# Kernel optimization log

Measured on AMD Instinct MI355X. Metric: run time of the kernel, lower is better.

## Reference

```python
import jax, jax.numpy as jnp
import numpy as np

B, E, H = 32768, 512, 512


def setup_inputs() -> dict:
    key = jax.random.key(0)
    ks = jax.random.split(key, 7)
    s_e = 1.0 / np.sqrt(E)
    s_h = 1.0 / np.sqrt(H)
    return {
        "input": jax.random.normal(ks[0], (B, E), jnp.float32),
        "h0": jax.random.normal(ks[1], (B, H), jnp.float32),
        "c0": jax.random.normal(ks[2], (B, H), jnp.float32),
        # stacked weights, gate order [i, f, o, g]
        "W_x": jax.random.uniform(ks[3], (4, H, E), jnp.float32, -s_e, s_e),
        "b_x": jax.random.uniform(ks[4], (4, H), jnp.float32, -s_e, s_e),
        "W_h": jax.random.uniform(ks[5], (4, H, H), jnp.float32, -s_h, s_h),
        "b_h": jax.random.uniform(ks[6], (4, H), jnp.float32, -s_h, s_h),
    }


def reference(input, h0, c0, W_x, b_x, W_h, b_h):
    # Fused: two GEMMs over stacked gate weights, then elementwise gate math.
    # z: [4, B, H]; gate order i, f, o, g
    z = (jnp.einsum('be,khe->kbh', input, W_x) + b_x[:, None, :]
         + jnp.einsum('bh,kgh->kbg', h0, W_h) + b_h[:, None, :])
    i = jax.nn.sigmoid(z[0])
    f = jax.nn.sigmoid(z[1])
    o = jax.nn.sigmoid(z[2])
    g = jnp.tanh(z[3])
    c1 = f * c0 + i * g
    h1 = o * jnp.tanh(c1)
    return (h1, c1)
```

## Files before the change

kernel.cpp:

```cpp
#include <hip/hip_runtime.h>


#define BQ 32768
#define HQ 512
#define KK 1024
#define BH (32768 * 512)

typedef __bf16 bf16x8 __attribute__((ext_vector_type(8)));
typedef float f32x4 __attribute__((ext_vector_type(4)));

__device__ __forceinline__ unsigned short f2bf(float f) {
    unsigned int u = __float_as_uint(f);
    unsigned int r = (u + 0x7fffu + ((u >> 16) & 1u)) >> 16;
    return (unsigned short)r;
}

__device__ __forceinline__ void gld_lds16(const unsigned short* g, unsigned short* l) {
    __builtin_amdgcn_global_load_lds(
        (const __attribute__((address_space(1))) void*)g,
        (__attribute__((address_space(3))) void*)l,
        16, 0, 0);
}

__device__ __forceinline__ bf16x8 cvt8(f32x4 a, f32x4 b) {
    bf16x8 w;
    w[0] = (__bf16)a[0]; w[1] = (__bf16)a[1]; w[2] = (__bf16)a[2]; w[3] = (__bf16)a[3];
    w[4] = (__bf16)b[0]; w[5] = (__bf16)b[1]; w[6] = (__bf16)b[2]; w[7] = (__bf16)b[3];
    return w;
}


__global__ __launch_bounds__(256) void pack_W(const float* __restrict__ Wx,
                                              const float* __restrict__ Wh,
                                              const float* __restrict__ bx,
                                              const float* __restrict__ bh,
                                              unsigned short* __restrict__ Wint,
                                              float* __restrict__ biasc) {
    int j = blockIdx.x * 256 + threadIdx.x;
    int c = j >> 8;
    int kc = (j & 255) * 4;
    int gate = (c >> 4) & 3;
    int h = ((c >> 6) << 4) + (c & 15);
    const float* src = (kc < 512)
        ? (Wx + ((size_t)gate * 512 + h) * 512 + kc)
        : (Wh + ((size_t)gate * 512 + h) * 512 + (kc - 512));
    float4 v = *(const float4*)src;
    ushort4 o;
    o.x = f2bf(v.x); o.y = f2bf(v.y); o.z = f2bf(v.z); o.w = f2bf(v.w);
    *(ushort4*)&Wint[(size_t)c * 1024 + kc] = o;
    if ((j & 255) == 0) biasc[c] = bx[gate * 512 + h] + bh[gate * 512 + h];
}


__global__ __launch_bounds__(256, 4) void lstm_gemm(const float* __restrict__ xin,
                                                    const float* __restrict__ hin,
                                                    const unsigned short* __restrict__ Wint,
                                                    const float* __restrict__ biasc,
                                                    const float* __restrict__ c0,
                                                    float* __restrict__ out) {
    __shared__ __align__(16) unsigned short ldsA[128 * 32];
    __shared__ __align__(16) unsigned short ldsB[128 * 32];

    const int tid = threadIdx.x;
    const int lane = tid & 63;
    const int wave = tid >> 6;
    const int wm = wave >> 1;
    const int wn = wave & 1;
    const int quad = lane >> 4;
    const int lrow = lane & 15;

    const int bn = blockIdx.x;
    const int bm = blockIdx.y;
    const int m0 = bm * 128;
    const int n0 = bn * 128;

    const int arow = tid >> 1;
    const int ahalf = tid & 1;
    const int aswz = (arow >> 1) & 3;
    const float* gAx = xin + (size_t)(m0 + arow) * HQ + ahalf * 16;
    const float* gAh = hin + (size_t)(m0 + arow) * HQ + ahalf * 16;
    unsigned short* wA0 = &ldsA[arow * 32 + (((ahalf * 2 + 0) ^ aswz) * 8)];
    unsigned short* wA1 = &ldsA[arow * 32 + (((ahalf * 2 + 1) ^ aswz) * 8)];

    const int brow = tid >> 2;
    const int bunit = (tid & 3) ^ ((tid >> 3) & 3);
    const unsigned short* gB = Wint + (size_t)(n0 + brow) * KK + bunit * 8;

    const int koff = (quad ^ ((lrow >> 1) & 3)) * 8;

    f32x4 acc[4][4];
    for (int i = 0; i < 4; i++)
        for (int j = 0; j < 4; j++) {
            f32x4 z = {0.f, 0.f, 0.f, 0.f};
            acc[i][j] = z;
        }

    f32x4 r0 = *(const f32x4*)(gAx + 0);
    f32x4 r1 = *(const f32x4*)(gAx + 4);
    f32x4 r2 = *(const f32x4*)(gAx + 8);
    f32x4 r3 = *(const f32x4*)(gAx + 12);

    for (int kt = 0; kt < KK; kt += 32) {
        gld_lds16(gB + kt, &ldsB[tid * 8]);
        gld_lds16(gB + (size_t)64 * KK + kt, &ldsB[2048 + tid * 8]);
        *(bf16x8*)wA0 = cvt8(r0, r1);
        *(bf16x8*)wA1 = cvt8(r2, r3);
        __syncthreads();

        const int kn = kt + 32;
        if (kn < KK) {
            const float* p = (kn < 512) ? (gAx + kn) : (gAh + (kn - 512));
            r0 = *(const f32x4*)(p + 0);
            r1 = *(const f32x4*)(p + 4);
            r2 = *(const f32x4*)(p + 8);
            r3 = *(const f32x4*)(p + 12);
        }

        bf16x8 af[4], bfr[4];
        for (int mi = 0; mi < 4; mi++)
            af[mi] = *(const bf16x8*)&ldsA[(wm * 64 + mi * 16 + lrow) * 32 + koff];
        for (int ni = 0; ni < 4; ni++)
            bfr[ni] = *(const bf16x8*)&ldsB[(wn * 64 + ni * 16 + lrow) * 32 + koff];
        for (int mi = 0; mi < 4; mi++)
            for (int ni = 0; ni < 4; ni++)
                acc[mi][ni] = __builtin_amdgcn_mfma_f32_16x16x32_bf16(
                    af[mi], bfr[ni], acc[mi][ni], 0, 0, 0);
        __syncthreads();
    }

    float bi[4];
    for (int ni = 0; ni < 4; ni++)
        bi[ni] = biasc[n0 + wn * 64 + ni * 16 + lrow];
    const int h = (bn * 2 + wn) * 16 + lrow;

    for (int mi = 0; mi < 4; mi++) {
        for (int r = 0; r < 4; r++) {
            int b = m0 + wm * 64 + mi * 16 + quad * 4 + r;
            float zi = acc[mi][0][r] + bi[0];
            float zf = acc[mi][1][r] + bi[1];
            float zo = acc[mi][2][r] + bi[2];
            float zg = acc[mi][3][r] + bi[3];
            float ig = 1.f / (1.f + __expf(-zi));
            float fg = 1.f / (1.f + __expf(-zf));
            float og = 1.f / (1.f + __expf(-zo));
            float gg = 1.f - 2.f / (__expf(2.f * zg) + 1.f);
            float c0v = c0[(size_t)b * HQ + h];
            float c1 = fg * c0v + ig * gg;
            float th = 1.f - 2.f / (__expf(2.f * c1) + 1.f);
            out[(size_t)b * HQ + h] = og * th;
            out[(size_t)BH + (size_t)b * HQ + h] = c1;
        }
    }
}

extern "C" void kernel_launch(void* const* d_in, const int* in_sizes, int n_in,
                              void* d_out, int out_size, void* d_ws, size_t ws_size,
                              hipStream_t stream) {
    (void)in_sizes; (void)n_in; (void)out_size; (void)ws_size;
    const float* input = (const float*)d_in[0];
    const float* h0    = (const float*)d_in[1];
    const float* c0    = (const float*)d_in[2];
    const float* Wx    = (const float*)d_in[3];
    const float* bx    = (const float*)d_in[4];
    const float* Wh    = (const float*)d_in[5];
    const float* bh    = (const float*)d_in[6];
    float* out = (float*)d_out;

    char* ws = (char*)d_ws;
    unsigned short* Wint = (unsigned short*)ws;
    float* biasc = (float*)(ws + (size_t)4 * 1024 * 1024);

    pack_W<<<2048, 256, 0, stream>>>(Wx, Wh, bx, bh, Wint, biasc);
    lstm_gemm<<<dim3(16, 256), 256, 0, stream>>>(input, h0, Wint, biasc, c0, out);
}
```

Baseline: 503.3 us.

## Double-buffer LDS tiles with one barrier per step and remap block order

Converts the GEMM main loop to double-buffered LDS, with a two-stage register prefetch of the fp32 A tile and async B loads into the alternate buffer. Each k-step now needs a single barrier, guarded by explicit waitcnt, so global loads overlap the MFMA work. The launch also changes to a 1D grid with an index remap that spreads M blocks across an interleaved order, which is meant to improve L2 reuse of the weight tiles. In exchange it doubles LDS use, adds register pressure from two A staging sets, and relies on hand-counted vmcnt values being correct.

After: 544.5 us. 1.08x slower.

```diff
diff --git a/kernel.cpp b/kernel.cpp
--- a/kernel.cpp
+++ b/kernel.cpp
@@ -27,6 +27,16 @@
     w[0] = (__bf16)a[0]; w[1] = (__bf16)a[1]; w[2] = (__bf16)a[2]; w[3] = (__bf16)a[3];
     w[4] = (__bf16)b[0]; w[5] = (__bf16)b[1]; w[6] = (__bf16)b[2]; w[7] = (__bf16)b[3];
     return w;
+}
+
+struct AR { f32x4 a, b, c, d; };
+
+__device__ __forceinline__ void loadA(const float* gAx, const float* gAh, int kt, AR& s) {
+    const float* p = (kt < 512) ? (gAx + kt) : (gAh + (kt - 512));
+    s.a = *(const f32x4*)(p + 0);
+    s.b = *(const f32x4*)(p + 4);
+    s.c = *(const f32x4*)(p + 8);
+    s.d = *(const f32x4*)(p + 12);
 }
 
 
@@ -58,8 +68,8 @@
                                                     const float* __restrict__ biasc,
                                                     const float* __restrict__ c0,
                                                     float* __restrict__ out) {
-    __shared__ __align__(16) unsigned short ldsA[128 * 32];
-    __shared__ __align__(16) unsigned short ldsB[128 * 32];
+    __shared__ __align__(16) unsigned short ldsA[2][128 * 32];
+    __shared__ __align__(16) unsigned short ldsB[2][128 * 32];
 
     const int tid = threadIdx.x;
     const int lane = tid & 63;
@@ -69,8 +79,10 @@
     const int quad = lane >> 4;
     const int lrow = lane & 15;
 
-    const int bn = blockIdx.x;
-    const int bm = blockIdx.y;
+    const int bid = blockIdx.x;
+    const int l = bid >> 3;
+    const int bm = (bid & 7) * 32 + (l >> 4);
+    const int bn = l & 15;
     const int m0 = bm * 128;
     const int n0 = bn * 128;
 
@@ -79,8 +91,8 @@
     const int aswz = (arow >> 1) & 3;
     const float* gAx = xin + (size_t)(m0 + arow) * HQ + ahalf * 16;
     const float* gAh = hin + (size_t)(m0 + arow) * HQ + ahalf * 16;
-    unsigned short* wA0 = &ldsA[arow * 32 + (((ahalf * 2 + 0) ^ aswz) * 8)];
-    unsigned short* wA1 = &ldsA[arow * 32 + (((ahalf * 2 + 1) ^ aswz) * 8)];
+    const int wa0 = arow * 32 + (((ahalf * 2 + 0) ^ aswz) * 8);
+    const int wa1 = arow * 32 + (((ahalf * 2 + 1) ^ aswz) * 8);
 
     const int brow = tid >> 2;
     const int bunit = (tid & 3) ^ ((tid >> 3) & 3);
@@ -95,37 +107,56 @@
             acc[i][j] = z;
         }
 
-    f32x4 r0 = *(const f32x4*)(gAx + 0);
-    f32x4 r1 = *(const f32x4*)(gAx + 4);
-    f32x4 r2 = *(const f32x4*)(gAx + 8);
-    f32x4 r3 = *(const f32x4*)(gAx + 12);
-
-    for (int kt = 0; kt < KK; kt += 32) {
-        gld_lds16(gB + kt, &ldsB[tid * 8]);
-        gld_lds16(gB + (size_t)64 * KK + kt, &ldsB[2048 + tid * 8]);
-        *(bf16x8*)wA0 = cvt8(r0, r1);
-        *(bf16x8*)wA1 = cvt8(r2, r3);
-        __syncthreads();
-
-        const int kn = kt + 32;
-        if (kn < KK) {
-            const float* p = (kn < 512) ? (gAx + kn) : (gAh + (kn - 512));
-            r0 = *(const f32x4*)(p + 0);
-            r1 = *(const f32x4*)(p + 4);
-            r2 = *(const f32x4*)(p + 8);
-            r3 = *(const f32x4*)(p + 12);
-        }
-
+    AR s0, s1;
+
+    loadA(gAx, gAh, 0, s0);
+    gld_lds16(gB, &ldsB[0][tid * 8]);
+    gld_lds16(gB + (size_t)64 * KK, &ldsB[0][2048 + tid * 8]);
+    *(bf16x8*)&ldsA[0][wa0] = cvt8(s0.a, s0.b);
+    *(bf16x8*)&ldsA[0][wa1] = cvt8(s0.c, s0.d);
+    loadA(gAx, gAh, 32, s1);
+    asm volatile("s_waitcnt vmcnt(4) lgkmcnt(0)" ::: "memory");
+    __builtin_amdgcn_s_barrier();
+
+#define STEP(I, CUR, WREG, LREG) do {                                          \
+    const int ktn_ = ((I) + 1) * 32;                                           \
+    gld_lds16(gB + ktn_, &ldsB[(CUR) ^ 1][tid * 8]);                           \
+    gld_lds16(gB + (size_t)64 * KK + ktn_, &ldsB[(CUR) ^ 1][2048 + tid * 8]);  \
+    bf16x8 af[4], bfr[4];                                                      \
+    for (int mi = 0; mi < 4; mi++)                                             \
+        af[mi] = *(const bf16x8*)&ldsA[CUR][(wm * 64 + mi * 16 + lrow) * 32 + koff]; \
+    for (int ni = 0; ni < 4; ni++)                                             \
+        bfr[ni] = *(const bf16x8*)&ldsB[CUR][(wn * 64 + ni * 16 + lrow) * 32 + koff]; \
+    *(bf16x8*)&ldsA[(CUR) ^ 1][wa0] = cvt8(WREG.a, WREG.b);                    \
+    *(bf16x8*)&ldsA[(CUR) ^ 1][wa1] = cvt8(WREG.c, WREG.d);                    \
+    int kt2_ = ((I) + 2) * 32;                                                 \
+    if (kt2_ >= KK) kt2_ = KK - 32;                                            \
+    loadA(gAx, gAh, kt2_, LREG);                                               \
+    for (int mi = 0; mi < 4; mi++)                                             \
+        for (int ni = 0; ni < 4; ni++)                                         \
+            acc[mi][ni] = __builtin_amdgcn_mfma_f32_16x16x32_bf16(             \
+                af[mi], bfr[ni], acc[mi][ni], 0, 0, 0);                        \
+    asm volatile("s_waitcnt vmcnt(4) lgkmcnt(0)" ::: "memory");                \
+    __builtin_amdgcn_s_barrier();                                              \
+} while (0)
+
+    for (int ii = 0; ii < 15; ++ii) {
+        STEP(2 * ii + 0, 0, s1, s0);
+        STEP(2 * ii + 1, 1, s0, s1);
+    }
+    STEP(30, 0, s1, s0);
+#undef STEP
+
+    {
         bf16x8 af[4], bfr[4];
         for (int mi = 0; mi < 4; mi++)
-            af[mi] = *(const bf16x8*)&ldsA[(wm * 64 + mi * 16 + lrow) * 32 + koff];
+            af[mi] = *(const bf16x8*)&ldsA[1][(wm * 64 + mi * 16 + lrow) * 32 + koff];
         for (int ni = 0; ni < 4; ni++)
-            bfr[ni] = *(const bf16x8*)&ldsB[(wn * 64 + ni * 16 + lrow) * 32 + koff];
+            bfr[ni] = *(const bf16x8*)&ldsB[1][(wn * 64 + ni * 16 + lrow) * 32 + koff];
         for (int mi = 0; mi < 4; mi++)
             for (int ni = 0; ni < 4; ni++)
                 acc[mi][ni] = __builtin_amdgcn_mfma_f32_16x16x32_bf16(
                     af[mi], bfr[ni], acc[mi][ni], 0, 0, 0);
-        __syncthreads();
     }
 
     float bi[4];
@@ -171,5 +202,5 @@
     float* biasc = (float*)(ws + (size_t)4 * 1024 * 1024);
 
     pack_W<<<2048, 256, 0, stream>>>(Wx, Wh, bx, bh, Wint, biasc);
-    lstm_gemm<<<dim3(16, 256), 256, 0, stream>>>(input, h0, Wint, biasc, c0, out);
-}
+    lstm_gemm<<<4096, 256, 0, stream>>>(input, h0, Wint, biasc, c0, out);
+}
```
